# Kernel optimization log

Measured on AMD Instinct MI355X. Metric: run time of the kernel, lower is better.

## Reference

```python
import jax, jax.numpy as jnp
import numpy as np

N, E, D = 50000, 512000, 128

def mish(x):
    return x * jnp.tanh(jax.nn.softplus(x))

def ln(x, g, b):
    m = jnp.mean(x, axis=-1, keepdims=True)
    v = jnp.var(x, axis=-1, keepdims=True)
    return (x - m) / jnp.sqrt(v + 1e-5) * g + b

def setup_inputs():
    key = jax.random.key(0)
    ks = jax.random.split(key, 16)
    W = lambda k, i, o: jax.random.normal(k, (i, o), jnp.float32) * 0.02
    z = jnp.zeros((D,), jnp.float32)
    o = jnp.ones((D,), jnp.float32)
    return {
        "node_feat": jax.random.normal(ks[0], (N, D), jnp.float32),
        "coord_feat": jax.random.normal(ks[1], (N, D), jnp.float32),
        "Wq": W(ks[2], D, D), "bq": z, "gq": o, "beq": z,
        "Wk": W(ks[3], D, D), "bk": z, "gk": o, "bek": z,
        "Wm1": W(ks[4], D, D), "bm1": z, "gm": o, "bem": z,
        "Wm2": W(ks[5], D, D), "bm2": z,
        "Wb1": W(ks[6], D, D), "bb1": z, "gb": o, "beb": z,
        "Wb2": W(ks[7], D, D), "bb2": z,
        "Ww1": W(ks[8], D, D), "bw1": z, "gw": o, "bew": z,
        "Ww2": W(ks[9], D, D), "bw2": z,
        "Wn1": W(ks[10], 2 * D, D), "bn1": z,
        "Wn2": W(ks[11], D, D), "bn2": z,
        "Wc1": W(ks[12], D, D), "bc1": z,
        "Wc2": W(ks[13], D, D),
        "src": jax.random.randint(ks[14], (E,), 0, N, jnp.int32),
        "dst": jax.random.randint(ks[15], (E,), 0, N, jnp.int32),
    }

def reference(node_feat, coord_feat, Wq, bq, gq, beq, Wk, bk, gk, bek,
              Wm1, bm1, gm, bem, Wm2, bm2, Wb1, bb1, gb, beb, Wb2, bb2,
              Ww1, bw1, gw, bew, Ww2, bw2, Wn1, bn1, Wn2, bn2, Wc1, bc1, Wc2,
              src, dst):
    # linear_q / linear_k on coord features: Linear -> LayerNorm -> Mish
    q = mish(ln(coord_feat @ Wq + bq, gq, beq))   # [N, D]
    k = mish(ln(coord_feat @ Wk + bk, gk, bek))   # [N, D]
    # u_sub_v('q','k'): per-edge q[src] - k[dst]
    rel = q[src] - k[dst]                          # [E, D]
    radial = jnp.sum(rel * rel, axis=-1, keepdims=True)  # [E, 1]
    rel = rel / jnp.sqrt(radial + 1e-8)
    # relative position encodings from dst coord features
    xd = coord_feat[dst]                           # [E, D]
    pem = mish(ln(xd @ Wm1 + bm1, gm, bem)) @ Wm2 + bm2
    peb = mish(ln(xd @ Wb1 + bb1, gb, beb)) @ Wb2 + bb2
    rel = rel * pem + peb
    # weight_encoding MLP
    w = mish(ln(rel @ Ww1 + bw1, gw, bew)) @ Ww2 + bw2  # [E, D]
    # dgl.softmax_edges over a single graph: softmax across the edge axis
    w = jax.nn.softmax(w, axis=0)
    # update_all(copy_e, sum): scatter-add edge weights to destination nodes
    h_neigh = jax.ops.segment_sum(w, dst, num_segments=N)  # [N, D]
    h = mish(jnp.concatenate([node_feat, h_neigh], axis=-1) @ Wn1 + bn1) @ Wn2 + bn2
    x = mish(coord_feat @ Wc1 + bc1) @ Wc2
    return (h, x)
```

## Files before the change

kernel.cpp:

```cpp
#include <hip/hip_runtime.h>
#include <cstdint>
#include <cstddef>

#define DN 128
#define NND 50000
#define NED 512000
#define NSCAN 49

typedef __attribute__((ext_vector_type(8))) short bf8;
typedef __attribute__((ext_vector_type(4))) float f4;
typedef unsigned short us;

__device__ __forceinline__ us f2bf(float f){
  union { float f; unsigned int u; } c; c.f = f;
  unsigned int r = c.u + 0x7fffu + ((c.u >> 16) & 1u);
  return (us)(r >> 16);
}
__device__ __forceinline__ float bf2f(us u){
  union { unsigned int u; float f; } c; c.u = ((unsigned int)u) << 16;
  return c.f;
}
__device__ __forceinline__ float mishf(float x){
  float e = __expf(x);
  float u = 1.f + e;
  float u2 = u * u;
  float t = (u2 - 1.f) / (u2 + 1.f);
  return x * ((x > 20.f) ? 1.f : t);
}

#define MFMA16(a, b, c) __builtin_amdgcn_mfma_f32_16x16x32_bf16((a), (b), (c), 0, 0, 0)

__device__ __forceinline__ bf8 lds_frag(const us* base, int row, int rowStrideB, int kElem){
  int byte = row * rowStrideB + kElem * 2;
  byte ^= (row & 7) << 4;
  return *(const bf8*)((const char*)base + byte);
}
__device__ __forceinline__ bf8 gfrag(const us* W, int n, int K, int kElem){
  return *(const bf8*)(W + (size_t)n * K + kElem);
}

template<int OUT_BF16>
__device__ __forceinline__ void store_tile(void* outp, int nrows, int r0,
                                           int wr, int wc, int g, int s, int ostride,
                                           const f4 (&A)[2][4]){
#pragma unroll
  for (int rt = 0; rt < 2; ++rt)
#pragma unroll
    for (int ct = 0; ct < 4; ++ct)
#pragma unroll
      for (int reg = 0; reg < 4; ++reg){
        int row = r0 + wr*32 + rt*16 + g*4 + reg;
        if (row < nrows){
          int col = wc*64 + ct*16 + s;
          float v = A[rt][ct][reg];
          if constexpr (OUT_BF16 != 0)
            ((us*)outp)[(size_t)row*ostride + col] = f2bf(v);
          else
            ((float*)outp)[(size_t)row*ostride + col] = v;
        }
      }
}

__device__ __forceinline__ void gemm_reg(const bf8 (&a)[2][4], const us* __restrict__ WT,
                                         const float* __restrict__ bias,
                                         int wc, int g, int s, f4 (&acc)[2][4]){
#pragma unroll
  for (int ct = 0; ct < 4; ++ct){
    float bv = bias ? bias[wc*64 + ct*16 + s] : 0.f;
    f4 t = {bv, bv, bv, bv};
    acc[0][ct] = t; acc[1][ct] = t;
  }
#pragma unroll
  for (int ct = 0; ct < 4; ++ct){
    int n = wc*64 + ct*16 + s;
#pragma unroll
    for (int kk = 0; kk < 4; ++kk){
      bf8 b = gfrag(WT, n, DN, kk*32 + g*8);
      acc[0][ct] = MFMA16(a[0][kk], b, acc[0][ct]);
      acc[1][ct] = MFMA16(a[1][kk], b, acc[1][ct]);
    }
  }
}

__device__ __forceinline__ void ln_mish(f4 (&acc)[2][4],
                                        const float* __restrict__ gam,
                                        const float* __restrict__ bet,
                                        int wr, int wc, int g, int s,
                                        float (*rowsum)[64][2], float (*rowsq)[64][2],
                                        int buf){
  float gv[4], bev[4];
#pragma unroll
  for (int ct = 0; ct < 4; ++ct){ int n = wc*64 + ct*16 + s; gv[ct] = gam[n]; bev[ct] = bet[n]; }
#pragma unroll
  for (int rt = 0; rt < 2; ++rt)
#pragma unroll
    for (int reg = 0; reg < 4; ++reg){
      float sm = acc[rt][0][reg] + acc[rt][1][reg] + acc[rt][2][reg] + acc[rt][3][reg];
      float sq = acc[rt][0][reg]*acc[rt][0][reg] + acc[rt][1][reg]*acc[rt][1][reg]
               + acc[rt][2][reg]*acc[rt][2][reg] + acc[rt][3][reg]*acc[rt][3][reg];
#pragma unroll
      for (int m = 1; m < 16; m <<= 1){ sm += __shfl_xor(sm, m, 64); sq += __shfl_xor(sq, m, 64); }
      if (s == 0){
        int row = wr*32 + rt*16 + g*4 + reg;
        rowsum[buf][row][wc] = sm; rowsq[buf][row][wc] = sq;
      }
    }
  __syncthreads();
#pragma unroll
  for (int rt = 0; rt < 2; ++rt)
#pragma unroll
    for (int reg = 0; reg < 4; ++reg){
      int row = wr*32 + rt*16 + g*4 + reg;
      float sm = rowsum[buf][row][0] + rowsum[buf][row][1];
      float sq = rowsq[buf][row][0] + rowsq[buf][row][1];
      float mu = sm * (1.f/128.f);
      float var = sq * (1.f/128.f) - mu*mu;
      float rs = rsqrtf(var + 1e-5f);
#pragma unroll
      for (int ct = 0; ct < 4; ++ct)
        acc[rt][ct][reg] = mishf((acc[rt][ct][reg] - mu) * rs * gv[ct] + bev[ct]);
    }
}

__device__ __forceinline__ void write_T(us* Tsh, int wr, int wc, int g, int s,
                                        const f4 (&A)[2][4]){
#pragma unroll
  for (int rt = 0; rt < 2; ++rt)
#pragma unroll
    for (int ct = 0; ct < 4; ++ct)
#pragma unroll
      for (int reg = 0; reg < 4; ++reg){
        int row = wr*32 + rt*16 + g*4 + reg;
        int col = wc*64 + ct*16 + s;
        int byte = row*256 + col*2; byte ^= (row & 7) << 4;
        *(us*)((char*)Tsh + byte) = f2bf(A[rt][ct][reg]);
      }
}

__device__ __forceinline__ void load_a2(const us* Tsh, int wr, int g, int s, bf8 (&a2)[2][4]){
#pragma unroll
  for (int rt = 0; rt < 2; ++rt)
#pragma unroll
    for (int kk = 0; kk < 4; ++kk)
      a2[rt][kk] = lds_frag(Tsh, wr*32 + rt*16 + s, 256, kk*32 + g*8);
}

__device__ __forceinline__ void loadA16(const us* T, int g, int s, bf8 (&a)[4]){
#pragma unroll
  for (int kk = 0; kk < 4; ++kk)
    a[kk] = lds_frag(T, s, 256, kk*32 + g*8);
}

__device__ __forceinline__ void gemm8(const bf8 (&a)[4], const us* __restrict__ WT,
                                      const float* __restrict__ bias,
                                      int g, int s, f4 (&acc)[8]){
#pragma unroll
  for (int ct = 0; ct < 8; ++ct){
    float bv = bias ? bias[ct*16 + s] : 0.f;
    f4 t = {bv, bv, bv, bv};
    acc[ct] = t;
  }
#pragma unroll
  for (int ct = 0; ct < 8; ++ct){
    int n = ct*16 + s;
#pragma unroll
    for (int kk = 0; kk < 4; ++kk)
      acc[ct] = MFMA16(a[kk], gfrag(WT, n, DN, kk*32 + g*8), acc[ct]);
  }
}

__device__ __forceinline__ void ln_mish8(f4 (&acc)[8],
                                         const float* __restrict__ gam,
                                         const float* __restrict__ bet, int s){
  float mu[4], rs[4];
#pragma unroll
  for (int reg = 0; reg < 4; ++reg){
    float sm = 0.f, sq = 0.f;
#pragma unroll
    for (int ct = 0; ct < 8; ++ct){ float v = acc[ct][reg]; sm += v; sq += v*v; }
#pragma unroll
    for (int m = 1; m < 16; m <<= 1){ sm += __shfl_xor(sm, m, 64); sq += __shfl_xor(sq, m, 64); }
    float mm = sm * (1.f/128.f);
    float var = sq * (1.f/128.f) - mm*mm;
    mu[reg] = mm; rs[reg] = rsqrtf(var + 1e-5f);
  }
#pragma unroll
  for (int ct = 0; ct < 8; ++ct){
    float gv = gam[ct*16 + s], bv = bet[ct*16 + s];
#pragma unroll
    for (int reg = 0; reg < 4; ++reg)
      acc[ct][reg] = mishf((acc[ct][reg] - mu[reg]) * rs[reg] * gv + bv);
  }
}

__device__ __forceinline__ void writeT16(us* T, int g, int s, const f4 (&A)[8]){
#pragma unroll
  for (int ct = 0; ct < 8; ++ct)
#pragma unroll
    for (int reg = 0; reg < 4; ++reg){
      int row = g*4 + reg, col = ct*16 + s;
      int byte = row*256 + col*2; byte ^= (row & 7) << 4;
      *(us*)((char*)T + byte) = f2bf(A[ct][reg]);
    }
}

__global__ __launch_bounds__(256, 2)
void node_fused(const float* __restrict__ X,
                const us* __restrict__ WqT,  const float* __restrict__ bq,
                const float* __restrict__ gq, const float* __restrict__ beq,
                const us* __restrict__ WkT,  const float* __restrict__ bk,
                const float* __restrict__ gk, const float* __restrict__ bek,
                const us* __restrict__ Wm1T, const float* __restrict__ bm1,
                const float* __restrict__ gm, const float* __restrict__ bem,
                const us* __restrict__ Wm2T, const float* __restrict__ bm2,
                const us* __restrict__ Wb1T, const float* __restrict__ bb1,
                const float* __restrict__ gb, const float* __restrict__ beb,
                const us* __restrict__ Wb2T, const float* __restrict__ bb2,
                const us* __restrict__ Wc1T, const float* __restrict__ bc1,
                const us* __restrict__ Wc2T,
                us* __restrict__ qt, us* __restrict__ kmb, float* __restrict__ xout)
{
  __shared__ us Ash[64 * DN];
  __shared__ float rowsum[2][64][2];
  __shared__ float rowsq[2][64][2];

  const int tid = threadIdx.x;
  const int r0 = blockIdx.x * 64;

  {
    int r = tid >> 2, c4 = tid & 3;
    int grow = r0 + r; if (grow >= NND) grow = NND - 1;
    const f4* sp = (const f4*)(X + (size_t)grow * DN + c4 * 32);
#pragma unroll
    for (int j = 0; j < 4; ++j){
      f4 v0 = sp[2*j], v1 = sp[2*j+1];
      bf8 o;
#pragma unroll
      for (int q = 0; q < 4; ++q){ o[q] = (short)f2bf(v0[q]); o[4+q] = (short)f2bf(v1[q]); }
      int byte = r*256 + c4*64 + j*16; byte ^= (r & 7) << 4;
      *(bf8*)((char*)Ash + byte) = o;
    }
  }
  __syncthreads();

  const int lane = tid & 63, w = tid >> 6;
  const int wr = w >> 1, wc = w & 1;
  const int g = lane >> 4, s = lane & 15;

  bf8 a[2][4];
#pragma unroll
  for (int rt = 0; rt < 2; ++rt)
#pragma unroll
    for (int kk = 0; kk < 4; ++kk)
      a[rt][kk] = lds_frag(Ash, wr*32 + rt*16 + s, 256, kk*32 + g*8);
  __syncthreads();

  f4 acc[2][4], acc2[2][4];
  bf8 a2[2][4];

  gemm_reg(a, WqT, bq, wc, g, s, acc);
  ln_mish(acc, gq, beq, wr, wc, g, s, rowsum, rowsq, 0);
  store_tile<1>((void*)qt, NND, r0, wr, wc, g, s, DN, acc);

  gemm_reg(a, WkT, bk, wc, g, s, acc);
  ln_mish(acc, gk, bek, wr, wc, g, s, rowsum, rowsq, 1);
  store_tile<1>((void*)kmb, NND, r0, wr, wc, g, s, 384, acc);

  gemm_reg(a, Wm1T, bm1, wc, g, s, acc);
  ln_mish(acc, gm, bem, wr, wc, g, s, rowsum, rowsq, 0);
  write_T(Ash, wr, wc, g, s, acc);
  __syncthreads();
  load_a2(Ash, wr, g, s, a2);
#pragma unroll
  for (int ct = 0; ct < 4; ++ct){
    float bv = bm2[wc*64 + ct*16 + s]; f4 t = {bv,bv,bv,bv}; acc2[0][ct] = t; acc2[1][ct] = t;
  }
#pragma unroll
  for (int ct = 0; ct < 4; ++ct){
    int n = wc*64 + ct*16 + s;
#pragma unroll
    for (int kk = 0; kk < 4; ++kk){
      bf8 b = gfrag(Wm2T, n, DN, kk*32 + g*8);
      acc2[0][ct] = MFMA16(a2[0][kk], b, acc2[0][ct]);
      acc2[1][ct] = MFMA16(a2[1][kk], b, acc2[1][ct]);
    }
  }
  store_tile<1>((void*)(kmb + 128), NND, r0, wr, wc, g, s, 384, acc2);

  gemm_reg(a, Wb1T, bb1, wc, g, s, acc);
  ln_mish(acc, gb, beb, wr, wc, g, s, rowsum, rowsq, 1);
  write_T(Ash, wr, wc, g, s, acc);
  __syncthreads();
  load_a2(Ash, wr, g, s, a2);
#pragma unroll
  for (int ct = 0; ct < 4; ++ct){
    float bv = bb2[wc*64 + ct*16 + s]; f4 t = {bv,bv,bv,bv}; acc2[0][ct] = t; acc2[1][ct] = t;
  }
#pragma unroll
  for (int ct = 0; ct < 4; ++ct){
    int n = wc*64 + ct*16 + s;
#pragma unroll
    for (int kk = 0; kk < 4; ++kk){
      bf8 b = gfrag(Wb2T, n, DN, kk*32 + g*8);
      acc2[0][ct] = MFMA16(a2[0][kk], b, acc2[0][ct]);
      acc2[1][ct] = MFMA16(a2[1][kk], b, acc2[1][ct]);
    }
  }
  store_tile<1>((void*)(kmb + 256), NND, r0, wr, wc, g, s, 384, acc2);

  gemm_reg(a, Wc1T, bc1, wc, g, s, acc);
#pragma unroll
  for (int rt = 0; rt < 2; ++rt)
#pragma unroll
    for (int ct = 0; ct < 4; ++ct)
#pragma unroll
      for (int reg = 0; reg < 4; ++reg)
        acc[rt][ct][reg] = mishf(acc[rt][ct][reg]);
  __syncthreads();
  write_T(Ash, wr, wc, g, s, acc);
  __syncthreads();
  load_a2(Ash, wr, g, s, a2);
#pragma unroll
  for (int ct = 0; ct < 4; ++ct){ f4 t = {0,0,0,0}; acc2[0][ct] = t; acc2[1][ct] = t; }
#pragma unroll
  for (int ct = 0; ct < 4; ++ct){
    int n = wc*64 + ct*16 + s;
#pragma unroll
    for (int kk = 0; kk < 4; ++kk){
      bf8 b = gfrag(Wc2T, n, DN, kk*32 + g*8);
      acc2[0][ct] = MFMA16(a2[0][kk], b, acc2[0][ct]);
      acc2[1][ct] = MFMA16(a2[1][kk], b, acc2[1][ct]);
    }
  }
  store_tile<0>((void*)xout, NND, r0, wr, wc, g, s, DN, acc2);
}

__global__ void csr_count(const int* __restrict__ dst, int* __restrict__ deg){
  int e = blockIdx.x * 256 + threadIdx.x;
  if (e < NED) atomicAdd(&deg[dst[e]], 1);
}

__global__ __launch_bounds__(1024) void csr_blocksum(const int* __restrict__ deg,
                                                     int* __restrict__ bsum){
  __shared__ int sb[1024];
  int t = threadIdx.x, idx = blockIdx.x * 1024 + t;
  sb[t] = (idx < NND) ? deg[idx] : 0;
  __syncthreads();
  for (int off = 512; off > 0; off >>= 1){
    if (t < off) sb[t] += sb[t + off];
    __syncthreads();
  }
  if (t == 0) bsum[blockIdx.x] = sb[0];
}

__global__ void csr_scanroot(const int* __restrict__ bsum, int* __restrict__ boff){
  if (threadIdx.x == 0){
    int run = 0;
    for (int b = 0; b < NSCAN; ++b){ boff[b] = run; run += bsum[b]; }
  }
}

__global__ __launch_bounds__(1024) void csr_scatter(const int* __restrict__ deg,
                                                    const int* __restrict__ boff,
                                                    int* __restrict__ fillctr){
  __shared__ int ss[1024];
  int t = threadIdx.x, idx = blockIdx.x * 1024 + t;
  int v = (idx < NND) ? deg[idx] : 0;
  ss[t] = v;
  __syncthreads();
  for (int off = 1; off < 1024; off <<= 1){
    int x = (t >= off) ? ss[t - off] : 0;
    __syncthreads();
    ss[t] += x;
    __syncthreads();
  }
  if (idx < NND){
    int p = boff[blockIdx.x] + ss[t] - v;
    fillctr[idx] = p;
  }
}

__global__ void csr_fill(const int* __restrict__ src, const int* __restrict__ dst,
                         int* __restrict__ fillctr,
                         int* __restrict__ ssorted, int* __restrict__ dsorted){
  int e = blockIdx.x * 256 + threadIdx.x;
  if (e < NED){
    int d = dst[e];
    int p = atomicAdd(&fillctr[d], 1);
    ssorted[p] = src[e];
    dsorted[p] = d;
  }
}

__global__ __launch_bounds__(256, 2)
void edge_kernel(const us* __restrict__ qtab,
                 const us* __restrict__ kmb,
                 const us* __restrict__ W1T,
                 const us* __restrict__ W2T,
                 const float* __restrict__ bw1,
                 const float* __restrict__ gwp,
                 const float* __restrict__ bewp,
                 const float* __restrict__ bw2,
                 const int* __restrict__ ssorted,
                 const int* __restrict__ dsorted,
                 float* __restrict__ hacc,
                 float* __restrict__ colsum8)
{
  __shared__ us Tsh[4][16 * DN];
  __shared__ int dsh[64];

  const int tid = threadIdx.x;
  const int lane = tid & 63, w = tid >> 6;
  const int g = lane >> 4, s = lane & 15;
  const int r = lane >> 2, c4 = lane & 3;

  const int nchunk = gridDim.x >> 3;
  const int swz = (blockIdx.x & 7) * nchunk + (blockIdx.x >> 3);
  const int e0 = swz * 64 + w * 16;
  us* T = (us*)Tsh[w];

  const int e = e0 + r;
  const int sn = ssorted[e], dn = dsorted[e];
  const bf8* qp = (const bf8*)(qtab + (size_t)sn * DN + c4 * 32);
  const us*  kb = kmb + (size_t)dn * 384 + c4 * 32;
  bf8 qv[4], kv[4], mv[4], bv[4];
#pragma unroll
  for (int j = 0; j < 4; ++j){
    qv[j] = qp[j];
    kv[j] = *(const bf8*)(kb + j*8);
    mv[j] = *(const bf8*)(kb + 128 + j*8);
    bv[j] = *(const bf8*)(kb + 256 + j*8);
  }
  if (c4 == 0) dsh[w*16 + r] = dn;

  float ss = 0.f;
#pragma unroll
  for (int j = 0; j < 4; ++j)
#pragma unroll
    for (int q = 0; q < 8; ++q){
      float d = bf2f((us)qv[j][q]) - bf2f((us)kv[j][q]);
      ss += d * d;
    }
  ss += __shfl_xor(ss, 1, 64);
  ss += __shfl_xor(ss, 2, 64);
  float rinv = rsqrtf(ss + 1e-8f);

#pragma unroll
  for (int j = 0; j < 4; ++j){
    bf8 o;
#pragma unroll
    for (int q = 0; q < 8; ++q){
      float d = bf2f((us)qv[j][q]) - bf2f((us)kv[j][q]);
      float v = d * rinv * bf2f((us)mv[j][q]) + bf2f((us)bv[j][q]);
      o[q] = (short)f2bf(v);
    }
    int byte = r*256 + c4*64 + j*16; byte ^= (r & 7) << 4;
    *(bf8*)((char*)T + byte) = o;
  }

  bf8 a[4];
  loadA16(T, g, s, a);
  f4 acc[8];
  gemm8(a, W1T, bw1, g, s, acc);
  ln_mish8(acc, gwp, bewp, s);
  writeT16(T, g, s, acc);
  bf8 a2[4];
  loadA16(T, g, s, a2);
  f4 p[8];
  gemm8(a2, W2T, bw2, g, s, p);
#pragma unroll
  for (int ct = 0; ct < 8; ++ct)
#pragma unroll
    for (int reg = 0; reg < 4; ++reg)
      p[ct][reg] = __expf(p[ct][reg]);

  writeT16(T, g, s, p);
  __syncthreads();

  {
    int col = tid & 127, half = tid >> 7;
    int rbeg = half * 32;
    float csum = 0.f;
    int prev = dsh[rbeg];
    float run = 0.f;
#pragma unroll 8
    for (int r2 = rbeg; r2 < rbeg + 32; ++r2){
      int qw = r2 >> 4, lr = r2 & 15;
      int byte = lr*256 + col*2; byte ^= (lr & 7) << 4;
      float v = bf2f(*(const us*)((const char*)Tsh[qw] + byte));
      int d = dsh[r2];
      csum += v;
      if (d != prev){
        atomicAdd(&hacc[(size_t)prev * DN + col], run);
        run = v; prev = d;
      } else {
        run += v;
      }
    }
    atomicAdd(&hacc[(size_t)prev * DN + col], run);
    atomicAdd(&colsum8[(blockIdx.x & 7) * DN + col], csum);
  }
}

__global__ __launch_bounds__(256, 2)
void final_h(const float* __restrict__ nodef,
             const float* __restrict__ hacc,
             const float* __restrict__ colsum8,
             const us* __restrict__ Wn1T,
             const float* __restrict__ bn1,
             const us* __restrict__ Wn2T,
             const float* __restrict__ bn2,
             float* __restrict__ outh)
{
  __shared__ us Ash[64 * 256];
  __shared__ float rcs[DN];

  const int tid = threadIdx.x;
  const int r0 = blockIdx.x * 64;

  if (tid < DN){
    float ssum = 0.f;
#pragma unroll
    for (int x = 0; x < 8; ++x) ssum += colsum8[x * DN + tid];
    rcs[tid] = 1.f / ssum;
  }
  __syncthreads();

  {
    int r = tid >> 2, c4 = tid & 3;
    int grow = r0 + r; if (grow >= NND) grow = NND - 1;
    const f4* np = (const f4*)(nodef + (size_t)grow * DN + c4 * 32);
    const f4* hp = (const f4*)(hacc + (size_t)grow * DN + c4 * 32);
#pragma unroll
    for (int j = 0; j < 4; ++j){
      f4 v0 = np[2*j], v1 = np[2*j+1];
      bf8 o;
#pragma unroll
      for (int q = 0; q < 4; ++q){ o[q] = (short)f2bf(v0[q]); o[4+q] = (short)f2bf(v1[q]); }
      int byte = r*512 + c4*64 + j*16; byte ^= (r & 7) << 4;
      *(bf8*)((char*)Ash + byte) = o;
      f4 h0 = hp[2*j], h1 = hp[2*j+1];
      bf8 o2;
#pragma unroll
      for (int q = 0; q < 4; ++q){
        o2[q]   = (short)f2bf(h0[q] * rcs[c4*32 + j*8 + q]);
        o2[4+q] = (short)f2bf(h1[q] * rcs[c4*32 + j*8 + 4 + q]);
      }
      int byte2 = r*512 + 256 + c4*64 + j*16; byte2 ^= (r & 7) << 4;
      *(bf8*)((char*)Ash + byte2) = o2;
    }
  }
  __syncthreads();

  const int lane = tid & 63, w = tid >> 6;
  const int wr = w >> 1, wc = w & 1;
  const int g = lane >> 4, s = lane & 15;

  float b1v[4], b2v[4];
#pragma unroll
  for (int ct = 0; ct < 4; ++ct){ int n = wc*64 + ct*16 + s; b1v[ct] = bn1[n]; b2v[ct] = bn2[n]; }

  f4 acc[2][4];
#pragma unroll
  for (int ct = 0; ct < 4; ++ct){ f4 t = {b1v[ct], b1v[ct], b1v[ct], b1v[ct]}; acc[0][ct] = t; acc[1][ct] = t; }

  bf8 a[2][8];
#pragma unroll
  for (int rt = 0; rt < 2; ++rt)
#pragma unroll
    for (int kk = 0; kk < 8; ++kk)
      a[rt][kk] = lds_frag(Ash, wr*32 + rt*16 + s, 512, kk*32 + g*8);
  __syncthreads();

#pragma unroll
  for (int ct = 0; ct < 4; ++ct){
    int n = wc*64 + ct*16 + s;
#pragma unroll
    for (int kk = 0; kk < 8; ++kk){
      bf8 b = gfrag(Wn1T, n, 256, kk*32 + g*8);
      acc[0][ct] = MFMA16(a[0][kk], b, acc[0][ct]);
      acc[1][ct] = MFMA16(a[1][kk], b, acc[1][ct]);
    }
  }

#pragma unroll
  for (int rt = 0; rt < 2; ++rt)
#pragma unroll
    for (int ct = 0; ct < 4; ++ct)
#pragma unroll
      for (int reg = 0; reg < 4; ++reg)
        acc[rt][ct][reg] = mishf(acc[rt][ct][reg]);
  write_T((us*)Ash, wr, wc, g, s, acc);
  __syncthreads();

  f4 acc2[2][4];
#pragma unroll
  for (int ct = 0; ct < 4; ++ct){ f4 t = {b2v[ct], b2v[ct], b2v[ct], b2v[ct]}; acc2[0][ct] = t; acc2[1][ct] = t; }
  bf8 a2[2][4];
  load_a2((const us*)Ash, wr, g, s, a2);
#pragma unroll
  for (int ct = 0; ct < 4; ++ct){
    int n = wc*64 + ct*16 + s;
#pragma unroll
    for (int kk = 0; kk < 4; ++kk){
      bf8 b = gfrag(Wn2T, n, DN, kk*32 + g*8);
      acc2[0][ct] = MFMA16(a2[0][kk], b, acc2[0][ct]);
      acc2[1][ct] = MFMA16(a2[1][kk], b, acc2[1][ct]);
    }
  }
  store_tile<0>((void*)outh, NND, r0, wr, wc, g, s, DN, acc2);
}

struct WPrepArgs {
  const float* w[12];
  us* wt[12];
  int K[12];
};

__global__ void prep_weights(WPrepArgs a){
  int widx = blockIdx.y;
  int K = a.K[widx];
  int idx = blockIdx.x * 256 + threadIdx.x;
  if (idx >= DN * K) return;
  int kshift = (K == 256) ? 8 : 7;
  int n = idx >> kshift;
  int k = idx & (K - 1);
  a.wt[widx][idx] = f2bf(a.w[widx][(size_t)k * DN + n]);
}

extern "C" void kernel_launch(void* const* d_in, const int* in_sizes, int n_in,
                              void* d_out, int out_size, void* d_ws, size_t ws_size,
                              hipStream_t stream) {
  const float* node_feat = (const float*)d_in[0];
  const float* coordf    = (const float*)d_in[1];
  const float* Wq  = (const float*)d_in[2];
  const float* bq  = (const float*)d_in[3];
  const float* gq  = (const float*)d_in[4];
  const float* beq = (const float*)d_in[5];
  const float* Wk  = (const float*)d_in[6];
  const float* bk  = (const float*)d_in[7];
  const float* gk  = (const float*)d_in[8];
  const float* bek = (const float*)d_in[9];
  const float* Wm1 = (const float*)d_in[10];
  const float* bm1 = (const float*)d_in[11];
  const float* gm  = (const float*)d_in[12];
  const float* bem = (const float*)d_in[13];
  const float* Wm2 = (const float*)d_in[14];
  const float* bm2 = (const float*)d_in[15];
  const float* Wb1 = (const float*)d_in[16];
  const float* bb1 = (const float*)d_in[17];
  const float* gb  = (const float*)d_in[18];
  const float* beb = (const float*)d_in[19];
  const float* Wb2 = (const float*)d_in[20];
  const float* bb2 = (const float*)d_in[21];
  const float* Ww1 = (const float*)d_in[22];
  const float* bw1 = (const float*)d_in[23];
  const float* gw  = (const float*)d_in[24];
  const float* bew = (const float*)d_in[25];
  const float* Ww2 = (const float*)d_in[26];
  const float* bw2 = (const float*)d_in[27];
  const float* Wn1 = (const float*)d_in[28];
  const float* bn1 = (const float*)d_in[29];
  const float* Wn2 = (const float*)d_in[30];
  const float* bn2 = (const float*)d_in[31];
  const float* Wc1 = (const float*)d_in[32];
  const float* bc1 = (const float*)d_in[33];
  const float* Wc2 = (const float*)d_in[34];
  const int* srcI  = (const int*)d_in[35];
  const int* dstI  = (const int*)d_in[36];

  char* ws = (char*)d_ws;
  size_t off = 0;
  auto alloc = [&](size_t bytes) -> char* {
    char* p = ws + off;
    off += (bytes + 255) & ~(size_t)255;
    return p;
  };
  us*    qt      = (us*)alloc((size_t)NND * DN * 2);
  us*    kmb     = (us*)alloc((size_t)NND * 384 * 2);
  float* hacc    = (float*)alloc((size_t)NND * DN * 4);
  float* colsum8 = (float*)alloc(8 * DN * 4);
  int*   deg     = (int*)alloc((size_t)NND * 4);
  int*   fillctr = (int*)alloc((size_t)NND * 4);
  int*   ssorted = (int*)alloc((size_t)NED * 4);
  int*   dsorted = (int*)alloc((size_t)NED * 4);
  int*   bsum    = (int*)alloc((size_t)NSCAN * 4);
  int*   boff    = (int*)alloc((size_t)NSCAN * 4);
  us*    wtb     = (us*)alloc((size_t)12 * 16384 * 2);

  hipMemsetAsync(hacc, 0, (size_t)NND * DN * 4 + 8 * DN * 4, stream);
  hipMemsetAsync(deg, 0, (size_t)NND * 4, stream);

  WPrepArgs pa;
  const float* wsrc[12] = {Wq, Wk, Wm1, Wm2, Wb1, Wb2, Ww1, Ww2, Wc1, Wc2, Wn2, Wn1};
  for (int i = 0; i < 12; ++i){
    pa.w[i] = wsrc[i];
    pa.wt[i] = wtb + (size_t)i * 16384;
    pa.K[i] = (i == 11) ? 256 : 128;
  }
  prep_weights<<<dim3(128, 12), 256, 0, stream>>>(pa);

  csr_count<<<(NED + 255) / 256, 256, 0, stream>>>(dstI, deg);
  csr_blocksum<<<NSCAN, 1024, 0, stream>>>(deg, bsum);
  csr_scanroot<<<1, 64, 0, stream>>>(bsum, boff);
  csr_scatter<<<NSCAN, 1024, 0, stream>>>(deg, boff, fillctr);
  csr_fill<<<(NED + 255) / 256, 256, 0, stream>>>(srcI, dstI, fillctr, ssorted, dsorted);

  const int NB = (NND + 63) / 64;

  node_fused<<<NB, 256, 0, stream>>>(coordf,
      pa.wt[0], bq, gq, beq,
      pa.wt[1], bk, gk, bek,
      pa.wt[2], bm1, gm, bem, pa.wt[3], bm2,
      pa.wt[4], bb1, gb, beb, pa.wt[5], bb2,
      pa.wt[8], bc1, pa.wt[9],
      qt, kmb, (float*)d_out + (size_t)NND * DN);

  edge_kernel<<<NED / 64, 256, 0, stream>>>(qt, kmb, pa.wt[6], pa.wt[7],
                                            bw1, gw, bew, bw2, ssorted, dsorted,
                                            hacc, colsum8);

  final_h<<<NB, 256, 0, stream>>>(node_feat, hacc, colsum8,
                                  pa.wt[11], bn1, pa.wt[10], bn2, (float*)d_out);
}
```

Baseline: 558.3 us.

## Process 32 edges per wave in edge kernel to reuse weight fragments

Each wave in the edge kernel now handles 32 edges (two 16-row MFMA tiles) instead of 16. Every weight fragment loaded from global memory feeds two MFMAs, which halves weight traffic per edge. The block-wide sync and cross-wave scatter are replaced by a per-wave segmented reduction in which each lane handles two columns, and colsum is spread over 16 slices to reduce atomic contention. Mish also uses fast division. Register and LDS use grow, which may lower occupancy, and the grid is halved.

```diff
diff --git a/kernel.cpp b/kernel.cpp
--- a/kernel.cpp
+++ b/kernel.cpp
@@ -24,7 +24,7 @@
   float e = __expf(x);
   float u = 1.f + e;
   float u2 = u * u;
-  float t = (u2 - 1.f) / (u2 + 1.f);
+  float t = __fdividef(u2 - 1.f, u2 + 1.f);
   return x * ((x > 20.f) ? 1.f : t);
 }
 
@@ -145,63 +145,73 @@
       a2[rt][kk] = lds_frag(Tsh, wr*32 + rt*16 + s, 256, kk*32 + g*8);
 }
 
-__device__ __forceinline__ void loadA16(const us* T, int g, int s, bf8 (&a)[4]){
-#pragma unroll
-  for (int kk = 0; kk < 4; ++kk)
-    a[kk] = lds_frag(T, s, 256, kk*32 + g*8);
-}
-
-__device__ __forceinline__ void gemm8(const bf8 (&a)[4], const us* __restrict__ WT,
-                                      const float* __restrict__ bias,
-                                      int g, int s, f4 (&acc)[8]){
+__device__ __forceinline__ void loadA32(const us* T, int g, int s, bf8 (&a)[2][4]){
+#pragma unroll
+  for (int rt = 0; rt < 2; ++rt)
+#pragma unroll
+    for (int kk = 0; kk < 4; ++kk)
+      a[rt][kk] = lds_frag(T, rt*16 + s, 256, kk*32 + g*8);
+}
+
+__device__ __forceinline__ void gemm32(const bf8 (&a)[2][4], const us* __restrict__ WT,
+                                       const float* __restrict__ bias,
+                                       int g, int s, f4 (&acc)[2][8]){
 #pragma unroll
   for (int ct = 0; ct < 8; ++ct){
     float bv = bias ? bias[ct*16 + s] : 0.f;
     f4 t = {bv, bv, bv, bv};
-    acc[ct] = t;
+    acc[0][ct] = t; acc[1][ct] = t;
   }
 #pragma unroll
   for (int ct = 0; ct < 8; ++ct){
     int n = ct*16 + s;
 #pragma unroll
-    for (int kk = 0; kk < 4; ++kk)
-      acc[ct] = MFMA16(a[kk], gfrag(WT, n, DN, kk*32 + g*8), acc[ct]);
-  }
-}
-
-__device__ __forceinline__ void ln_mish8(f4 (&acc)[8],
-                                         const float* __restrict__ gam,
-                                         const float* __restrict__ bet, int s){
-  float mu[4], rs[4];
-#pragma unroll
-  for (int reg = 0; reg < 4; ++reg){
-    float sm = 0.f, sq = 0.f;
-#pragma unroll
-    for (int ct = 0; ct < 8; ++ct){ float v = acc[ct][reg]; sm += v; sq += v*v; }
-#pragma unroll
-    for (int m = 1; m < 16; m <<= 1){ sm += __shfl_xor(sm, m, 64); sq += __shfl_xor(sq, m, 64); }
-    float mm = sm * (1.f/128.f);
-    float var = sq * (1.f/128.f) - mm*mm;
-    mu[reg] = mm; rs[reg] = rsqrtf(var + 1e-5f);
-  }
-#pragma unroll
-  for (int ct = 0; ct < 8; ++ct){
-    float gv = gam[ct*16 + s], bv = bet[ct*16 + s];
-#pragma unroll
-    for (int reg = 0; reg < 4; ++reg)
-      acc[ct][reg] = mishf((acc[ct][reg] - mu[reg]) * rs[reg] * gv + bv);
-  }
-}
-
-__device__ __forceinline__ void writeT16(us* T, int g, int s, const f4 (&A)[8]){
-#pragma unroll
-  for (int ct = 0; ct < 8; ++ct)
+    for (int kk = 0; kk < 4; ++kk){
+      bf8 b = gfrag(WT, n, DN, kk*32 + g*8);
+      acc[0][ct] = MFMA16(a[0][kk], b, acc[0][ct]);
+      acc[1][ct] = MFMA16(a[1][kk], b, acc[1][ct]);
+    }
+  }
+}
+
+__device__ __forceinline__ void ln_mish32(f4 (&acc)[2][8],
+                                          const float* __restrict__ gam,
+                                          const float* __restrict__ bet, int s){
+#pragma unroll
+  for (int rt = 0; rt < 2; ++rt){
+    float mu[4], rs[4];
 #pragma unroll
     for (int reg = 0; reg < 4; ++reg){
-      int row = g*4 + reg, col = ct*16 + s;
-      int byte = row*256 + col*2; byte ^= (row & 7) << 4;
-      *(us*)((char*)T + byte) = f2bf(A[ct][reg]);
-    }
+      float sm = 0.f, sq = 0.f;
+#pragma unroll
+      for (int ct = 0; ct < 8; ++ct){ float v = acc[rt][ct][reg]; sm += v; sq += v*v; }
+#pragma unroll
+      for (int m = 1; m < 16; m <<= 1){ sm += __shfl_xor(sm, m, 64); sq += __shfl_xor(sq, m, 64); }
+      float mm = sm * (1.f/128.f);
+      float var = sq * (1.f/128.f) - mm*mm;
+      mu[reg] = mm; rs[reg] = rsqrtf(var + 1e-5f);
+    }
+#pragma unroll
+    for (int ct = 0; ct < 8; ++ct){
+      float gv = gam[ct*16 + s], bv = bet[ct*16 + s];
+#pragma unroll
+      for (int reg = 0; reg < 4; ++reg)
+        acc[rt][ct][reg] = mishf((acc[rt][ct][reg] - mu[reg]) * rs[reg] * gv + bv);
+    }
+  }
+}
+
+__device__ __forceinline__ void writeT32(us* T, int g, int s, const f4 (&A)[2][8]){
+#pragma unroll
+  for (int rt = 0; rt < 2; ++rt)
+#pragma unroll
+    for (int ct = 0; ct < 8; ++ct)
+#pragma unroll
+      for (int reg = 0; reg < 4; ++reg){
+        int row = rt*16 + g*4 + reg, col = ct*16 + s;
+        int byte = row*256 + col*2; byte ^= (row & 7) << 4;
+        *(us*)((char*)T + byte) = f2bf(A[rt][ct][reg]);
+      }
 }
 
 __global__ __launch_bounds__(256, 2)
@@ -404,10 +414,10 @@
                  const int* __restrict__ ssorted,
                  const int* __restrict__ dsorted,
                  float* __restrict__ hacc,
-                 float* __restrict__ colsum8)
+                 float* __restrict__ colsum16)
 {
-  __shared__ us Tsh[4][16 * DN];
-  __shared__ int dsh[64];
+  __shared__ us Tsh[4][32 * DN];
+  __shared__ int dsh[4][32];
 
   const int tid = threadIdx.x;
   const int lane = tid & 63, w = tid >> 6;
@@ -416,96 +426,104 @@
 
   const int nchunk = gridDim.x >> 3;
   const int swz = (blockIdx.x & 7) * nchunk + (blockIdx.x >> 3);
-  const int e0 = swz * 64 + w * 16;
+  const int e0w = swz * 128 + w * 32;
   us* T = (us*)Tsh[w];
-
-  const int e = e0 + r;
-  const int sn = ssorted[e], dn = dsorted[e];
-  const bf8* qp = (const bf8*)(qtab + (size_t)sn * DN + c4 * 32);
-  const us*  kb = kmb + (size_t)dn * 384 + c4 * 32;
-  bf8 qv[4], kv[4], mv[4], bv[4];
-#pragma unroll
-  for (int j = 0; j < 4; ++j){
-    qv[j] = qp[j];
-    kv[j] = *(const bf8*)(kb + j*8);
-    mv[j] = *(const bf8*)(kb + 128 + j*8);
-    bv[j] = *(const bf8*)(kb + 256 + j*8);
-  }
-  if (c4 == 0) dsh[w*16 + r] = dn;
-
-  float ss = 0.f;
-#pragma unroll
-  for (int j = 0; j < 4; ++j)
-#pragma unroll
-    for (int q = 0; q < 8; ++q){
-      float d = bf2f((us)qv[j][q]) - bf2f((us)kv[j][q]);
-      ss += d * d;
-    }
-  ss += __shfl_xor(ss, 1, 64);
-  ss += __shfl_xor(ss, 2, 64);
-  float rinv = rsqrtf(ss + 1e-8f);
-
-#pragma unroll
-  for (int j = 0; j < 4; ++j){
-    bf8 o;
-#pragma unroll
-    for (int q = 0; q < 8; ++q){
-      float d = bf2f((us)qv[j][q]) - bf2f((us)kv[j][q]);
-      float v = d * rinv * bf2f((us)mv[j][q]) + bf2f((us)bv[j][q]);
-      o[q] = (short)f2bf(v);
-    }
-    int byte = r*256 + c4*64 + j*16; byte ^= (r & 7) << 4;
-    *(bf8*)((char*)T + byte) = o;
-  }
-
-  bf8 a[4];
-  loadA16(T, g, s, a);
-  f4 acc[8];
-  gemm8(a, W1T, bw1, g, s, acc);
-  ln_mish8(acc, gwp, bewp, s);
-  writeT16(T, g, s, acc);
-  bf8 a2[4];
-  loadA16(T, g, s, a2);
-  f4 p[8];
-  gemm8(a2, W2T, bw2, g, s, p);
-#pragma unroll
-  for (int ct = 0; ct < 8; ++ct)
-#pragma unroll
-    for (int reg = 0; reg < 4; ++reg)
-      p[ct][reg] = __expf(p[ct][reg]);
-
-  writeT16(T, g, s, p);
-  __syncthreads();
+  int* dloc = dsh[w];
+
+#pragma unroll
+  for (int hh = 0; hh < 2; ++hh){
+    int e = e0w + hh*16 + r;
+    int sn = ssorted[e], dn = dsorted[e];
+    const bf8* qp = (const bf8*)(qtab + (size_t)sn * DN + c4 * 32);
+    const us*  kb = kmb + (size_t)dn * 384 + c4 * 32;
+    bf8 qv[4], kv[4], mv[4], bv[4];
+#pragma unroll
+    for (int j = 0; j < 4; ++j){
+      qv[j] = qp[j];
+      kv[j] = *(const bf8*)(kb + j*8);
+      mv[j] = *(const bf8*)(kb + 128 + j*8);
+      bv[j] = *(const bf8*)(kb + 256 + j*8);
+    }
+    if (c4 == 0) dloc[hh*16 + r] = dn;
+
+    float ss = 0.f;
+#pragma unroll
+    for (int j = 0; j < 4; ++j)
+#pragma unroll
+      for (int q = 0; q < 8; ++q){
+        float d = bf2f((us)qv[j][q]) - bf2f((us)kv[j][q]);
+        ss += d * d;
+      }
+    ss += __shfl_xor(ss, 1, 64);
+    ss += __shfl_xor(ss, 2, 64);
+    float rinv = rsqrtf(ss + 1e-8f);
+
+    int lrow = hh*16 + r;
+#pragma unroll
+    for (int j = 0; j < 4; ++j){
+      bf8 o;
+#pragma unroll
+      for (int q = 0; q < 8; ++q){
+        float d = bf2f((us)qv[j][q]) - bf2f((us)kv[j][q]);
+        float v = d * rinv * bf2f((us)mv[j][q]) + bf2f((us)bv[j][q]);
+        o[q] = (short)f2bf(v);
+      }
+      int byte = lrow*256 + c4*64 + j*16; byte ^= (lrow & 7) << 4;
+      *(bf8*)((char*)T + byte) = o;
+    }
+  }
+
+  bf8 a[2][4];
+  loadA32(T, g, s, a);
+  f4 acc[2][8];
+  gemm32(a, W1T, bw1, g, s, acc);
+  ln_mish32(acc, gwp, bewp, s);
+  writeT32(T, g, s, acc);
+  bf8 a2[2][4];
+  loadA32(T, g, s, a2);
+  gemm32(a2, W2T, bw2, g, s, acc);
+#pragma unroll
+  for (int rt = 0; rt < 2; ++rt)
+#pragma unroll
+    for (int ct = 0; ct < 8; ++ct)
+#pragma unroll
+      for (int reg = 0; reg < 4; ++reg)
+        acc[rt][ct][reg] = __expf(acc[rt][ct][reg]);
+
+  writeT32(T, g, s, acc);
 
   {
-    int col = tid & 127, half = tid >> 7;
-    int rbeg = half * 32;
-    float csum = 0.f;
-    int prev = dsh[rbeg];
-    float run = 0.f;
+    int cA = lane * 2;
+    float run0 = 0.f, run1 = 0.f, cs0 = 0.f, cs1 = 0.f;
+    int prev = dloc[0];
 #pragma unroll 8
-    for (int r2 = rbeg; r2 < rbeg + 32; ++r2){
-      int qw = r2 >> 4, lr = r2 & 15;
-      int byte = lr*256 + col*2; byte ^= (lr & 7) << 4;
-      float v = bf2f(*(const us*)((const char*)Tsh[qw] + byte));
-      int d = dsh[r2];
-      csum += v;
+    for (int r2 = 0; r2 < 32; ++r2){
+      int byte = r2*256 + cA*2; byte ^= (r2 & 7) << 4;
+      unsigned int v = *(const unsigned int*)((const char*)T + byte);
+      float f0 = bf2f((us)(v & 0xffffu));
+      float f1 = bf2f((us)(v >> 16));
+      int d = dloc[r2];
+      cs0 += f0; cs1 += f1;
       if (d != prev){
-        atomicAdd(&hacc[(size_t)prev * DN + col], run);
-        run = v; prev = d;
+        atomicAdd(&hacc[(size_t)prev * DN + cA], run0);
+        atomicAdd(&hacc[(size_t)prev * DN + cA + 1], run1);
+        run0 = f0; run1 = f1; prev = d;
       } else {
-        run += v;
+        run0 += f0; run1 += f1;
       }
     }
-    atomicAdd(&hacc[(size_t)prev * DN + col], run);
-    atomicAdd(&colsum8[(blockIdx.x & 7) * DN + col], csum);
+    atomicAdd(&hacc[(size_t)prev * DN + cA], run0);
+    atomicAdd(&hacc[(size_t)prev * DN + cA + 1], run1);
+    int slice = ((blockIdx.x & 7) << 1) | (w & 1);
+    atomicAdd(&colsum16[slice * DN + cA], cs0);
+    atomicAdd(&colsum16[slice * DN + cA + 1], cs1);
   }
 }
 
 __global__ __launch_bounds__(256, 2)
 void final_h(const float* __restrict__ nodef,
              const float* __restrict__ hacc,
-             const float* __restrict__ colsum8,
+             const float* __restrict__ colsum16,
              const us* __restrict__ Wn1T,
              const float* __restrict__ bn1,
              const us* __restrict__ Wn2T,
@@ -521,7 +539,7 @@
   if (tid < DN){
     float ssum = 0.f;
 #pragma unroll
-    for (int x = 0; x < 8; ++x) ssum += colsum8[x * DN + tid];
+    for (int x = 0; x < 16; ++x) ssum += colsum16[x * DN + tid];
     rcs[tid] = 1.f / ssum;
   }
   __syncthreads();
@@ -676,19 +694,19 @@
     off += (bytes + 255) & ~(size_t)255;
     return p;
   };
-  us*    qt      = (us*)alloc((size_t)NND * DN * 2);
-  us*    kmb     = (us*)alloc((size_t)NND * 384 * 2);
-  float* hacc    = (float*)alloc((size_t)NND * DN * 4);
-  float* colsum8 = (float*)alloc(8 * DN * 4);
-  int*   deg     = (int*)alloc((size_t)NND * 4);
-  int*   fillctr = (int*)alloc((size_t)NND * 4);
-  int*   ssorted = (int*)alloc((size_t)NED * 4);
-  int*   dsorted = (int*)alloc((size_t)NED * 4);
-  int*   bsum    = (int*)alloc((size_t)NSCAN * 4);
-  int*   boff    = (int*)alloc((size_t)NSCAN * 4);
-  us*    wtb     = (us*)alloc((size_t)12 * 16384 * 2);
-
-  hipMemsetAsync(hacc, 0, (size_t)NND * DN * 4 + 8 * DN * 4, stream);
+  us*    qt       = (us*)alloc((size_t)NND * DN * 2);
+  us*    kmb      = (us*)alloc((size_t)NND * 384 * 2);
+  float* hacc     = (float*)alloc((size_t)NND * DN * 4);
+  float* colsum16 = (float*)alloc(16 * DN * 4);
+  int*   deg      = (int*)alloc((size_t)NND * 4);
+  int*   fillctr  = (int*)alloc((size_t)NND * 4);
+  int*   ssorted  = (int*)alloc((size_t)NED * 4);
+  int*   dsorted  = (int*)alloc((size_t)NED * 4);
+  int*   bsum     = (int*)alloc((size_t)NSCAN * 4);
+  int*   boff     = (int*)alloc((size_t)NSCAN * 4);
+  us*    wtb      = (us*)alloc((size_t)13 * 16384 * 2);
+
+  hipMemsetAsync(hacc, 0, (size_t)NND * DN * 4 + 16 * DN * 4, stream);
   hipMemsetAsync(deg, 0, (size_t)NND * 4, stream);
 
   WPrepArgs pa;
@@ -716,10 +734,10 @@
       pa.wt[8], bc1, pa.wt[9],
       qt, kmb, (float*)d_out + (size_t)NND * DN);
 
-  edge_kernel<<<NED / 64, 256, 0, stream>>>(qt, kmb, pa.wt[6], pa.wt[7],
-                                            bw1, gw, bew, bw2, ssorted, dsorted,
-                                            hacc, colsum8);
-
-  final_h<<<NB, 256, 0, stream>>>(node_feat, hacc, colsum8,
+  edge_kernel<<<NED / 128, 256, 0, stream>>>(qt, kmb, pa.wt[6], pa.wt[7],
+                                             bw1, gw, bew, bw2, ssorted, dsorted,
+                                             hacc, colsum16);
+
+  final_h<<<NB, 256, 0, stream>>>(node_feat, hacc, colsum16,
                                   pa.wt[11], bn1, pa.wt[10], bn2, (float*)d_out);
 }
```

After: 522.1 us. -6.5%, faster.
